# Kernel optimization log

Hardware: AMD Instinct MI355X
Metric: run time of the kernel (lower is better)

Reference implementation:

```python
import jax, jax.numpy as jnp
import numpy as np

N_NODES = 100000
N_HEDGES = 30000
N_PINS = 400000
D = 128          # hidden_channels
H = 4            # heads
K = D // H       # per-head dim
N_BLOCKS = 4     # n_layers=2, each layer = (vertex2edge, edge2vertex)
LN_EPS = 1e-5


def setup_inputs() -> dict:
    key = jax.random.key(0)
    ks = jax.random.split(key, 10)
    s = 1.0 / np.sqrt(D)
    return {
        "x_0": jax.random.normal(ks[0], (N_NODES, D), jnp.float32),
        "Kw": jax.random.normal(ks[1], (N_BLOCKS, H, D, K), jnp.float32) * s,
        "Vw": jax.random.normal(ks[2], (N_BLOCKS, H, D, K), jnp.float32) * s,
        "Qw": jax.random.normal(ks[3], (N_BLOCKS, H, K), jnp.float32) * s,
        "W1": jax.random.normal(ks[4], (N_BLOCKS, D, D), jnp.float32) * s,
        "b1": jnp.zeros((N_BLOCKS, D), jnp.float32),
        "W2": jax.random.normal(ks[5], (N_BLOCKS, D, D), jnp.float32) * s,
        "b2": jnp.zeros((N_BLOCKS, D), jnp.float32),
        "ln0_g": jnp.ones((N_BLOCKS, D), jnp.float32),
        "ln0_b": jnp.zeros((N_BLOCKS, D), jnp.float32),
        "ln1_g": jnp.ones((N_BLOCKS, D), jnp.float32),
        "ln1_b": jnp.zeros((N_BLOCKS, D), jnp.float32),
        "node_idx": jax.random.randint(ks[6], (N_PINS,), 0, N_NODES),
        "hedge_idx": jax.random.randint(ks[7], (N_PINS,), 0, N_HEDGES),
        "n_hyperedges": N_HEDGES,
    }


def _ln(x, g, b):
    mu = jnp.mean(x, -1, keepdims=True)
    var = jnp.mean((x - mu) ** 2, -1, keepdims=True)
    return (x - mu) * jax.lax.rsqrt(var + LN_EPS) * g + b


def _segment_softmax(logits, seg, num_segments):
    # softmax over incident pins grouped by target (sparse softmax over source dim)
    m = jax.ops.segment_max(logits, seg, num_segments=num_segments)
    ex = jnp.exp(logits - m[seg])
    denom = jax.ops.segment_sum(ex, seg, num_segments=num_segments)
    return ex / denom[seg]


def _block(x_src, src, tgt, n_tgt, Kw, Vw, Qw, W1, b1, W2, b2, g0, be0, g1, be1):
    # Multi-head PMA attention with a single learned query per head.
    Kx = jnp.einsum('nd,hdk->nhk', x_src, Kw)           # [n_src, H, K]
    Vx = jnp.einsum('nd,hdk->nhk', x_src, Vw)           # [n_src, H, K]
    logits = jnp.einsum('hk,nhk->nh', Qw, Kx)           # [n_src, H]
    w = _segment_softmax(logits[src], tgt, n_tgt)       # [E, H]
    msg = (w[:, :, None] * Vx[src]).reshape(-1, H * K)  # [E, D] head-concat
    agg = jax.ops.segment_sum(msg, tgt, num_segments=n_tgt)  # [n_tgt, D]
    x = _ln(agg + Qw.reshape(1, H * K), g0, be0)        # Q skip + LN0
    h = jnp.maximum(x @ W1 + b1, 0.0) @ W2 + b2         # 2-layer MLP
    return _ln(x + h, g1, be1)                          # residual + LN1


def reference(x_0, Kw, Vw, Qw, W1, b1, W2, b2, ln0_g, ln0_b, ln1_g, ln1_b,
              node_idx, hedge_idx, n_hyperedges):
    n_nodes = x_0.shape[0]
    x0, x1 = x_0, None
    for layer in range(N_BLOCKS // 2):
        bv, bev = 2 * layer, 2 * layer + 1
        # vertex -> hyperedge
        x1 = jax.nn.relu(_block(x0, node_idx, hedge_idx, n_hyperedges,
                                Kw[bv], Vw[bv], Qw[bv], W1[bv], b1[bv], W2[bv], b2[bv],
                                ln0_g[bv], ln0_b[bv], ln1_g[bv], ln1_b[bv]))
        # hyperedge -> vertex
        x0 = jax.nn.relu(_block(x1, hedge_idx, node_idx, n_nodes,
                                Kw[bev], Vw[bev], Qw[bev], W1[bev], b1[bev], W2[bev], b2[bev],
                                ln0_g[bev], ln0_b[bev], ln1_g[bev], ln1_b[bev]))
    return (x0, x1)
```

## Files before the change

kernel.cpp:

```cpp
#include <hip/hip_runtime.h>

#define N_NODES 100000
#define N_HEDGES 30000
#define N_PINS 400000
#define NPN 100096
#define NPH 30080
#define OVF_CAP 8192

typedef __attribute__((ext_vector_type(8))) short bf16x8;
typedef __attribute__((ext_vector_type(4))) float f32x4;
typedef unsigned short ushort_t;

__device__ __forceinline__ unsigned short f2bf(float f) {
  unsigned int u = __float_as_uint(f);
  u += 0x7FFF + ((u >> 16) & 1);
  return (unsigned short)(u >> 16);
}
__device__ __forceinline__ float bf2f(unsigned short s) {
  return __uint_as_float(((unsigned int)s) << 16);
}
__device__ __forceinline__ void gload16(const void* g, void* l) {
  __builtin_amdgcn_global_load_lds(
      (const __attribute__((address_space(1))) unsigned int*)g,
      (__attribute__((address_space(3))) unsigned int*)l, 16, 0, 0);
}

__global__ __launch_bounds__(256) void prep_k(
    const float* __restrict__ Kw, const float* __restrict__ Vw,
    const float* __restrict__ Qw, const float* __restrict__ W1,
    const float* __restrict__ W2, ushort_t* __restrict__ Vvqsw,
    ushort_t* __restrict__ W1sw, ushort_t* __restrict__ W2sw) {
  int i = blockIdx.x * 256 + threadIdx.x;
  if (i < 4 * 144 * 128) {
    int b = i / 18432, r = i % 18432, c = r >> 7, d = r & 127;
    float v;
    if (c < 128) {
      v = Vw[((b * 4 + (c >> 5)) * 128 + d) * 32 + (c & 31)];
    } else if (c < 132) {
      int h = c - 128;
      const float* kp = Kw + ((b * 4 + h) * 128 + d) * 32;
      const float* qp = Qw + (b * 4 + h) * 32;
      float s = 0.f;
      for (int k = 0; k < 32; ++k) s += kp[k] * qp[k];
      v = s;
    } else {
      v = 0.f;
    }
    int L = (c * 256 + d * 2) ^ ((c & 7) << 4);
    Vvqsw[b * 18432 + L / 2] = f2bf(v);
  }
  if (i < 4 * 128 * 128) {
    int b = i >> 14, r = i & 16383, c = r >> 7, k = r & 127;
    int L = (c * 256 + k * 2) ^ ((c & 7) << 4);
    int idx = b * 16384 + L / 2;
    W1sw[idx] = f2bf(W1[b * 16384 + k * 128 + c]);
    W2sw[idx] = f2bf(W2[b * 16384 + k * 128 + c]);
  }
}

__global__ __launch_bounds__(256) void conv_k(const float* __restrict__ x,
                                              ushort_t* __restrict__ xb, int n4) {
  int i = blockIdx.x * 256 + threadIdx.x;
  if (i < n4) {
    float4 v = ((const float4*)x)[i];
    ushort_t o0 = f2bf(v.x), o1 = f2bf(v.y), o2 = f2bf(v.z), o3 = f2bf(v.w);
    ushort_t* p = xb + (size_t)i * 4;
    p[0] = o0; p[1] = o1; p[2] = o2; p[3] = o3;
  }
}

__global__ __launch_bounds__(256) void csr_count(
    const int* __restrict__ node_idx, const int* __restrict__ hedge_idx,
    int* __restrict__ cntN, int* __restrict__ cntH) {
  int e = blockIdx.x * 256 + threadIdx.x;
  if (e < N_PINS) {
    atomicAdd(&cntN[node_idx[e]], 1);
    atomicAdd(&cntH[hedge_idx[e]], 1);
  }
}

__global__ __launch_bounds__(256) void csr_scan(
    const int* __restrict__ cnt, int* __restrict__ start, int2* __restrict__ seg,
    int n, int* gctr, int thresh, int* __restrict__ ovf, int* __restrict__ ovfcnt) {
  __shared__ int wsum[4];
  __shared__ int bbase;
  int i = blockIdx.x * 256 + threadIdx.x;
  int lane = threadIdx.x & 63, wid = threadIdx.x >> 6;
  int v = (i < n) ? cnt[i] : 0;
  int sc = v;
#pragma unroll
  for (int s = 1; s < 64; s <<= 1) {
    int tv = __shfl_up(sc, s);
    if (lane >= s) sc += tv;
  }
  if (lane == 63) wsum[wid] = sc;
  __syncthreads();
  if (threadIdx.x == 0) {
    int s0 = wsum[0], s1 = wsum[1], s2 = wsum[2], s3 = wsum[3];
    wsum[0] = 0; wsum[1] = s0; wsum[2] = s0 + s1; wsum[3] = s0 + s1 + s2;
    bbase = atomicAdd(gctr, s0 + s1 + s2 + s3);
  }
  __syncthreads();
  if (i < n) {
    int st = bbase + wsum[wid] + (sc - v);
    start[i] = st;
    seg[i] = make_int2(st, v);
    if (v > thresh) {
      int k = atomicAdd(ovfcnt, 1);
      if (k < OVF_CAP) ovf[k] = i;
    }
  }
}

__global__ __launch_bounds__(256) void csr_fill(
    const int* __restrict__ node_idx, const int* __restrict__ hedge_idx,
    const int* __restrict__ startN, const int* __restrict__ startH,
    int* __restrict__ fillN, int* __restrict__ fillH,
    int* __restrict__ pinsN, int* __restrict__ pinsH) {
  int e = blockIdx.x * 256 + threadIdx.x;
  if (e < N_PINS) {
    int n = node_idx[e], h = hedge_idx[e];
    int pH = startH[h] + atomicAdd(&fillH[h], 1);
    pinsH[pH] = n;
    int pN = startN[n] + atomicAdd(&fillN[n], 1);
    pinsN[pN] = h;
  }
}

__global__ __launch_bounds__(256) void transform_k(
    const ushort_t* __restrict__ xb, const ushort_t* __restrict__ Bsw,
    ushort_t* __restrict__ Vxb, float* __restrict__ lg, int n) {
  __shared__ char Blds[36864];
  __shared__ char Olds[16384];
  int t = threadIdx.x, l = t & 63, w = t >> 6;
  size_t r0 = (size_t)blockIdx.x * 64;
#pragma unroll
  for (int it = 0; it < 9; ++it) {
    int off = it * 4096 + w * 1024 + l * 16;
    gload16((const char*)Bsw + off, Blds + off);
  }
  __syncthreads();

  f32x4 acc[9];
#pragma unroll
  for (int ct = 0; ct < 9; ++ct) acc[ct] = (f32x4){0.f, 0.f, 0.f, 0.f};
  int swz = (l & 7) << 4;
  int lbase = (l & 15) * 256 + (l >> 4) * 16;
  const ushort_t* abase = xb + (r0 + w * 16 + (l & 15)) * 128 + (l >> 4) * 8;
#pragma unroll
  for (int kk = 0; kk < 4; ++kk) {
    bf16x8 a = *(const bf16x8*)(abase + kk * 32);
#pragma unroll
    for (int ct = 0; ct < 9; ++ct) {
      bf16x8 b = *(const bf16x8*)(Blds + ((ct * 4096 + kk * 64 + lbase) ^ swz));
      acc[ct] = __builtin_amdgcn_mfma_f32_16x16x32_bf16(a, b, acc[ct], 0, 0, 0);
    }
  }
  if ((l & 15) < 4) {
    size_t rb = r0 + w * 16 + (l >> 4) * 4;
#pragma unroll
    for (int j = 0; j < 4; ++j) lg[(rb + j) * 4 + (l & 15)] = acc[8][j];
  }
  int row64 = w * 16 + (l >> 4) * 4;
#pragma unroll
  for (int ct = 0; ct < 8; ++ct) {
    int c2 = (ct * 16 + (l & 15)) * 2;
#pragma unroll
    for (int j = 0; j < 4; ++j) {
      int r = row64 + j;
      int addr = (r * 256 + c2) ^ ((r & 0xC) << 3);
      *(ushort_t*)(Olds + addr) = f2bf(acc[ct][j]);
    }
  }
  __syncthreads();
#pragma unroll
  for (int it = 0; it < 4; ++it) {
    int L = it * 4096 + t * 16;
    int r = L >> 8;
    int phys = L ^ ((r & 0xC) << 3);
    *(uint4*)((char*)Vxb + r0 * 256 + L) = *(const uint4*)(Olds + phys);
  }
}

template <int L>
__global__ __launch_bounds__(256) void attn_g(
    const ushort_t* __restrict__ Vxb, const float* __restrict__ lg,
    const int2* __restrict__ seg, const int* __restrict__ pins,
    const float* __restrict__ Qflat, const float* __restrict__ g0,
    const float* __restrict__ be0, ushort_t* __restrict__ xmidb, int n_tgt,
    int mainBlocks, const int* __restrict__ ovf, const int* __restrict__ ovfcnt) {
  constexpr int G = 64 / L;
  constexpr int C = 128 / L;
  __shared__ float wl[4][G][L][4];
  __shared__ int pl[4][G][L];
  int wid = threadIdx.x >> 6, lane = threadIdx.x & 63;
  const char* vb = (const char*)Vxb;

  if ((int)blockIdx.x < mainBlocks) {
    int g = lane / L, li = lane % L;
    int tg = ((int)blockIdx.x * 4 + wid) * G + g;
    bool tval = tg < n_tgt;
    int2 sc = tval ? seg[tg] : make_int2(0, 0);
    int base = sc.x, deg = sc.y;
    bool fast = deg <= L;
    int mydeg = (tval && fast) ? deg : 0;
    bool act = li < mydeg;
    int p = act ? pins[base + li] : 0;
    float4 l4;
    if (act) l4 = *(const float4*)(lg + p * 4);
    else l4 = make_float4(-3.4e38f, -3.4e38f, -3.4e38f, -3.4e38f);
    float m0 = l4.x, m1 = l4.y, m2 = l4.z, m3 = l4.w;
#pragma unroll
    for (int off = 1; off < L; off <<= 1) {
      m0 = fmaxf(m0, __shfl_xor(m0, off));
      m1 = fmaxf(m1, __shfl_xor(m1, off));
      m2 = fmaxf(m2, __shfl_xor(m2, off));
      m3 = fmaxf(m3, __shfl_xor(m3, off));
    }
    float e0 = __expf(l4.x - m0), e1 = __expf(l4.y - m1);
    float e2 = __expf(l4.z - m2), e3 = __expf(l4.w - m3);
    float s0 = e0, s1 = e1, s2 = e2, s3 = e3;
#pragma unroll
    for (int off = 1; off < L; off <<= 1) {
      s0 += __shfl_xor(s0, off);
      s1 += __shfl_xor(s1, off);
      s2 += __shfl_xor(s2, off);
      s3 += __shfl_xor(s3, off);
    }
    wl[wid][g][li][0] = e0 / s0;
    wl[wid][g][li][1] = e1 / s1;
    wl[wid][g][li][2] = e2 / s2;
    wl[wid][g][li][3] = e3 / s3;
    pl[wid][g][li] = p << 8;

    int myh = li / (L / 4);
    float acc[C];
#pragma unroll
    for (int c = 0; c < C; ++c) acc[c] = 0.f;
    for (int e = 0; e < mydeg; ++e) {
      int off = pl[wid][g][e];
      float wgt = wl[wid][g][e][myh];
      const char* src = vb + off + li * (C * 2);
      unsigned u[C / 2];
      if constexpr (C == 8) {
        uint4 v = *(const uint4*)src;
        u[0] = v.x; u[1] = v.y; u[2] = v.z; u[3] = v.w;
      } else {
        uint2 v = *(const uint2*)src;
        u[0] = v.x; u[1] = v.y;
      }
#pragma unroll
      for (int j = 0; j < C / 2; ++j) {
        acc[2 * j] = fmaf(wgt, __uint_as_float(u[j] << 16), acc[2 * j]);
        acc[2 * j + 1] = fmaf(wgt, __uint_as_float(u[j] & 0xffff0000u), acc[2 * j + 1]);
      }
    }
    float q[C], gv[C], bv[C];
#pragma unroll
    for (int j = 0; j < C / 4; ++j) {
      float4 t = *(const float4*)(Qflat + li * C + j * 4);
      q[j * 4] = t.x; q[j * 4 + 1] = t.y; q[j * 4 + 2] = t.z; q[j * 4 + 3] = t.w;
      t = *(const float4*)(g0 + li * C + j * 4);
      gv[j * 4] = t.x; gv[j * 4 + 1] = t.y; gv[j * 4 + 2] = t.z; gv[j * 4 + 3] = t.w;
      t = *(const float4*)(be0 + li * C + j * 4);
      bv[j * 4] = t.x; bv[j * 4 + 1] = t.y; bv[j * 4 + 2] = t.z; bv[j * 4 + 3] = t.w;
    }
    float t1 = 0.f, t2 = 0.f;
#pragma unroll
    for (int c = 0; c < C; ++c) {
      float x = acc[c] + q[c];
      acc[c] = x;
      t1 += x;
      t2 += x * x;
    }
#pragma unroll
    for (int off = 1; off < L; off <<= 1) {
      t1 += __shfl_xor(t1, off);
      t2 += __shfl_xor(t2, off);
    }
    float mean = t1 * (1.f / 128.f);
    float var = t2 * (1.f / 128.f) - mean * mean;
    float rs = rsqrtf(var + 1e-5f);
    if (tval && fast) {
      float o[C];
#pragma unroll
      for (int c = 0; c < C; ++c) o[c] = (acc[c] - mean) * rs * gv[c] + bv[c];
      char* dst = (char*)xmidb + (size_t)tg * 256 + li * (C * 2);
      if constexpr (C == 8) {
        uint4 pk;
        pk.x = ((unsigned)f2bf(o[1]) << 16) | f2bf(o[0]);
        pk.y = ((unsigned)f2bf(o[3]) << 16) | f2bf(o[2]);
        pk.z = ((unsigned)f2bf(o[5]) << 16) | f2bf(o[4]);
        pk.w = ((unsigned)f2bf(o[7]) << 16) | f2bf(o[6]);
        *(uint4*)dst = pk;
      } else {
        uint2 pk;
        pk.x = ((unsigned)f2bf(o[1]) << 16) | f2bf(o[0]);
        pk.y = ((unsigned)f2bf(o[3]) << 16) | f2bf(o[2]);
        *(uint2*)dst = pk;
      }
    }
    return;
  }

  int cnt = *ovfcnt;
  if (cnt > OVF_CAP) cnt = OVF_CAP;
  int head = lane >> 4;
  for (int idx = ((int)blockIdx.x - mainBlocks) * 4 + wid; idx < cnt; idx += 128) {
    int tg = ovf[idx];
    int2 sc = seg[tg];
    int base = sc.x, deg = sc.y;
    float m0 = -3.4e38f, m1 = -3.4e38f, m2 = -3.4e38f, m3 = -3.4e38f;
    for (int i = lane; i < deg; i += 64) {
      int p = pins[base + i];
      float4 l4 = *(const float4*)(lg + p * 4);
      m0 = fmaxf(m0, l4.x); m1 = fmaxf(m1, l4.y);
      m2 = fmaxf(m2, l4.z); m3 = fmaxf(m3, l4.w);
    }
#pragma unroll
    for (int off = 1; off < 64; off <<= 1) {
      m0 = fmaxf(m0, __shfl_xor(m0, off));
      m1 = fmaxf(m1, __shfl_xor(m1, off));
      m2 = fmaxf(m2, __shfl_xor(m2, off));
      m3 = fmaxf(m3, __shfl_xor(m3, off));
    }
    float s0 = 0.f, s1 = 0.f, s2 = 0.f, s3 = 0.f;
    for (int i = lane; i < deg; i += 64) {
      int p = pins[base + i];
      float4 l4 = *(const float4*)(lg + p * 4);
      s0 += __expf(l4.x - m0); s1 += __expf(l4.y - m1);
      s2 += __expf(l4.z - m2); s3 += __expf(l4.w - m3);
    }
#pragma unroll
    for (int off = 1; off < 64; off <<= 1) {
      s0 += __shfl_xor(s0, off);
      s1 += __shfl_xor(s1, off);
      s2 += __shfl_xor(s2, off);
      s3 += __shfl_xor(s3, off);
    }
    float mh = (head & 2) ? ((head & 1) ? m3 : m2) : ((head & 1) ? m1 : m0);
    float sh = (head & 2) ? ((head & 1) ? s3 : s2) : ((head & 1) ? s1 : s0);
    float rdh = (deg > 0) ? 1.f / sh : 0.f;
    float acc0 = 0.f, acc1 = 0.f;
    for (int e = 0; e < deg; ++e) {
      int p = pins[base + e];
      float w0 = __expf(lg[p * 4 + head] - mh) * rdh;
      unsigned int v = *(const unsigned int*)(vb + (p << 8) + lane * 4);
      acc0 = fmaf(w0, __uint_as_float(v << 16), acc0);
      acc1 = fmaf(w0, __uint_as_float(v & 0xffff0000u), acc1);
    }
    float2 q2 = ((const float2*)Qflat)[lane];
    float x0v = acc0 + q2.x;
    float x1v = acc1 + q2.y;
    float t1 = x0v + x1v, t2 = x0v * x0v + x1v * x1v;
#pragma unroll
    for (int off = 1; off < 64; off <<= 1) {
      t1 += __shfl_xor(t1, off);
      t2 += __shfl_xor(t2, off);
    }
    float mean = t1 * (1.f / 128.f);
    float var = t2 * (1.f / 128.f) - mean * mean;
    float rs = rsqrtf(var + 1e-5f);
    float2 gg = ((const float2*)g0)[lane];
    float2 bb = ((const float2*)be0)[lane];
    float o0 = (x0v - mean) * rs * gg.x + bb.x;
    float o1 = (x1v - mean) * rs * gg.y + bb.y;
    unsigned int pk = ((unsigned int)f2bf(o1) << 16) | f2bf(o0);
    ((unsigned int*)xmidb)[tg * 64 + lane] = pk;
  }
}

__global__ __launch_bounds__(256) void mlp_k(
    const ushort_t* __restrict__ xmb, const ushort_t* __restrict__ W1sw,
    const float* __restrict__ b1, const ushort_t* __restrict__ W2sw,
    const float* __restrict__ b2, const float* __restrict__ g1,
    const float* __restrict__ be1, float* __restrict__ outf,
    ushort_t* __restrict__ outb, int n, int wf32) {
  __shared__ char Wlds[32768];
  __shared__ char Hlds[16384];
  int t = threadIdx.x, l = t & 63, w = t >> 6;
  size_t r0 = (size_t)blockIdx.x * 64;
#pragma unroll
  for (int it = 0; it < 8; ++it) {
    int off = it * 4096 + w * 1024 + l * 16;
    gload16((const char*)W1sw + off, Wlds + off);
  }
  float b1v[8], b2v[8], g1v[8], be1v[8];
#pragma unroll
  for (int ct = 0; ct < 8; ++ct) {
    int c = ct * 16 + (l & 15);
    b1v[ct] = b1[c]; b2v[ct] = b2[c]; g1v[ct] = g1[c]; be1v[ct] = be1[c];
  }
  __syncthreads();

  int swz = (l & 7) << 4;
  int lbase = (l & 15) * 256 + (l >> 4) * 16;
  f32x4 acc[8];
#pragma unroll
  for (int ct = 0; ct < 8; ++ct) acc[ct] = (f32x4){b1v[ct], b1v[ct], b1v[ct], b1v[ct]};
  const ushort_t* abase = xmb + (r0 + w * 16 + (l & 15)) * 128 + (l >> 4) * 8;
#pragma unroll
  for (int kk = 0; kk < 4; ++kk) {
    bf16x8 a = *(const bf16x8*)(abase + kk * 32);
#pragma unroll
    for (int ct = 0; ct < 8; ++ct) {
      bf16x8 b = *(const bf16x8*)(Wlds + ((ct * 4096 + kk * 64 + lbase) ^ swz));
      acc[ct] = __builtin_amdgcn_mfma_f32_16x16x32_bf16(a, b, acc[ct], 0, 0, 0);
    }
  }
  int hbase = w * 4096;
#pragma unroll
  for (int ct = 0; ct < 8; ++ct) {
    int c2 = (ct * 16 + (l & 15)) * 2;
#pragma unroll
    for (int j = 0; j < 4; ++j) {
      int rl = (l >> 4) * 4 + j;
      int addr = hbase + ((rl * 256 + c2) ^ ((rl & 7) << 4));
      *(ushort_t*)(Hlds + addr) = f2bf(fmaxf(acc[ct][j], 0.f));
    }
  }
  __syncthreads();
#pragma unroll
  for (int it = 0; it < 8; ++it) {
    int off = it * 4096 + w * 1024 + l * 16;
    gload16((const char*)W2sw + off, Wlds + off);
  }
  __syncthreads();

  f32x4 acc2[8];
#pragma unroll
  for (int ct = 0; ct < 8; ++ct) acc2[ct] = (f32x4){b2v[ct], b2v[ct], b2v[ct], b2v[ct]};
#pragma unroll
  for (int kk = 0; kk < 4; ++kk) {
    bf16x8 a = *(const bf16x8*)(Hlds + (hbase + ((lbase + kk * 64) ^ swz)));
#pragma unroll
    for (int ct = 0; ct < 8; ++ct) {
      bf16x8 b = *(const bf16x8*)(Wlds + ((ct * 4096 + kk * 64 + lbase) ^ swz));
      acc2[ct] = __builtin_amdgcn_mfma_f32_16x16x32_bf16(a, b, acc2[ct], 0, 0, 0);
    }
  }
  size_t rbase = r0 + w * 16 + (l >> 4) * 4;
  float s1[4] = {0.f, 0.f, 0.f, 0.f}, s2[4] = {0.f, 0.f, 0.f, 0.f};
#pragma unroll
  for (int ct = 0; ct < 8; ++ct) {
    int c = ct * 16 + (l & 15);
#pragma unroll
    for (int j = 0; j < 4; ++j) {
      float x = bf2f(xmb[(rbase + j) * 128 + c]);
      float y = acc2[ct][j] + x;
      acc2[ct][j] = y;
      s1[j] += y;
      s2[j] += y * y;
    }
  }
#pragma unroll
  for (int off = 1; off < 16; off <<= 1) {
#pragma unroll
    for (int j = 0; j < 4; ++j) {
      s1[j] += __shfl_xor(s1[j], off);
      s2[j] += __shfl_xor(s2[j], off);
    }
  }
  float mean[4], rs[4];
#pragma unroll
  for (int j = 0; j < 4; ++j) {
    mean[j] = s1[j] * (1.f / 128.f);
    float var = s2[j] * (1.f / 128.f) - mean[j] * mean[j];
    rs[j] = rsqrtf(var + 1e-5f);
  }
#pragma unroll
  for (int ct = 0; ct < 8; ++ct) {
    int c = ct * 16 + (l & 15);
#pragma unroll
    for (int j = 0; j < 4; ++j) {
      float o = fmaxf((acc2[ct][j] - mean[j]) * rs[j] * g1v[ct] + be1v[ct], 0.f);
      size_t row = rbase + j;
      outb[row * 128 + c] = f2bf(o);
      if (wf32 && row < (size_t)n) outf[row * 128 + c] = o;
    }
  }
}

extern "C" void kernel_launch(void* const* d_in, const int* in_sizes, int n_in,
                              void* d_out, int out_size, void* d_ws, size_t ws_size,
                              hipStream_t stream) {
  const float* x0_in = (const float*)d_in[0];
  const float* Kw  = (const float*)d_in[1];
  const float* Vw  = (const float*)d_in[2];
  const float* Qw  = (const float*)d_in[3];
  const float* W1  = (const float*)d_in[4];
  const float* b1  = (const float*)d_in[5];
  const float* W2  = (const float*)d_in[6];
  const float* b2  = (const float*)d_in[7];
  const float* ln0g = (const float*)d_in[8];
  const float* ln0b = (const float*)d_in[9];
  const float* ln1g = (const float*)d_in[10];
  const float* ln1b = (const float*)d_in[11];
  const int* node_idx  = (const int*)d_in[12];
  const int* hedge_idx = (const int*)d_in[13];

  float* out = (float*)d_out;
  float* x0_out = out;
  float* x1_out = out + (size_t)N_NODES * 128;

  char* w = (char*)d_ws;
  auto alloc = [&](size_t bytes) -> void* {
    void* p = (void*)w;
    w += (bytes + 255) & ~(size_t)255;
    return p;
  };
  ushort_t* Vvqsw = (ushort_t*)alloc(4 * 18432 * 2);
  ushort_t* W1sw  = (ushort_t*)alloc(4 * 16384 * 2);
  ushort_t* W2sw  = (ushort_t*)alloc(4 * 16384 * 2);
  ushort_t* x0b   = (ushort_t*)alloc((size_t)NPN * 128 * 2);
  ushort_t* x1b   = (ushort_t*)alloc((size_t)NPH * 128 * 2);
  ushort_t* Vxb   = (ushort_t*)alloc((size_t)NPN * 128 * 2);
  float*    lg    = (float*)alloc((size_t)NPN * 4 * 4);
  ushort_t* xmidb = (ushort_t*)alloc((size_t)NPN * 128 * 2);
  int* startH = (int*)alloc(N_HEDGES * 4);
  int* startN = (int*)alloc(N_NODES * 4);
  int2* segH  = (int2*)alloc((size_t)N_HEDGES * 8);
  int2* segN  = (int2*)alloc((size_t)N_NODES * 8);
  int* pinsH  = (int*)alloc(N_PINS * 4);
  int* pinsN  = (int*)alloc(N_PINS * 4);
  int* ovfH   = (int*)alloc(OVF_CAP * 4);
  int* ovfN   = (int*)alloc(OVF_CAP * 4);
  int* zbase  = (int*)alloc((size_t)(2 * (N_HEDGES + N_NODES) + 4) * 4);
  int* cntH = zbase;
  int* cntN = cntH + N_HEDGES;
  int* fillH = cntN + N_NODES;
  int* fillN = fillH + N_HEDGES;
  int* gctr = fillN + N_NODES;

  hipMemsetAsync(zbase, 0, (size_t)(2 * (N_HEDGES + N_NODES) + 4) * 4, stream);

  conv_k<<<(N_NODES * 128 / 4 + 255) / 256, 256, 0, stream>>>(x0_in, x0b, N_NODES * 32);
  prep_k<<<288, 256, 0, stream>>>(Kw, Vw, Qw, W1, W2, Vvqsw, W1sw, W2sw);
  csr_count<<<(N_PINS + 255) / 256, 256, 0, stream>>>(node_idx, hedge_idx, cntN, cntH);
  csr_scan<<<(N_HEDGES + 255) / 256, 256, 0, stream>>>(cntH, startH, segH, N_HEDGES,
                                                       gctr + 0, 32, ovfH, gctr + 2);
  csr_scan<<<(N_NODES + 255) / 256, 256, 0, stream>>>(cntN, startN, segN, N_NODES,
                                                      gctr + 1, 16, ovfN, gctr + 3);
  csr_fill<<<(N_PINS + 255) / 256, 256, 0, stream>>>(node_idx, hedge_idx, startN, startH,
                                                     fillN, fillH, pinsN, pinsH);

  const ushort_t* srcs[4] = {x0b, x1b, x0b, x1b};
  int n_srcs[4] = {N_NODES, N_HEDGES, N_NODES, N_HEDGES};
  const int2* segs[4] = {segH, segN, segH, segN};
  const int* pinss[4] = {pinsH, pinsN, pinsH, pinsN};
  int n_tgts[4] = {N_HEDGES, N_NODES, N_HEDGES, N_NODES};
  float* outf[4] = {x1_out, x0_out, x1_out, x0_out};
  ushort_t* outbs[4] = {x1b, x0b, x1b, x0b};
  int wf32[4] = {0, 0, 1, 1};

  const int mbH = (N_HEDGES + 7) / 8;
  const int mbN = (N_NODES + 15) / 16;

  for (int b = 0; b < 4; ++b) {
    int n_src = n_srcs[b], n_tgt = n_tgts[b];
    transform_k<<<(n_src + 63) / 64, 256, 0, stream>>>(srcs[b], Vvqsw + b * 18432,
                                                       Vxb, lg, n_src);
    if (b & 1) {
      attn_g<16><<<mbN + 32, 256, 0, stream>>>(Vxb, lg, segs[b], pinss[b],
                                               Qw + b * 128, ln0g + b * 128,
                                               ln0b + b * 128, xmidb, n_tgt,
                                               mbN, ovfN, gctr + 3);
    } else {
      attn_g<32><<<mbH + 32, 256, 0, stream>>>(Vxb, lg, segs[b], pinss[b],
                                               Qw + b * 128, ln0g + b * 128,
                                               ln0b + b * 128, xmidb, n_tgt,
                                               mbH, ovfH, gctr + 2);
    }
    mlp_k<<<(n_tgt + 63) / 64, 256, 0, stream>>>(xmidb, W1sw + b * 16384, b1 + b * 128,
                                                 W2sw + b * 16384, b2 + b * 128,
                                                 ln1g + b * 128, ln1b + b * 128,
                                                 outf[b], outbs[b], n_tgt, wf32[b]);
  }
}
```

Baseline: 315.6 us.

## Fuse preprocessing kernels and reuse count-atomic ranks for CSR fill

Merges the bf16 conversion, CSR counting and weight prep into one grid-stride kernel, and merges the two scans into one launch. The per-pin rank returned by the counting atomics is saved as a packed 16-bit pair, so the fill step no longer needs a second round of atomics or the fill counters. The last block also skips writing the unused bf16 output. This cuts launch count and atomic traffic. The packed ranks assume fewer than 65536 pins per segment.

```diff
diff --git a/kernel.cpp b/kernel.cpp
--- a/kernel.cpp
+++ b/kernel.cpp
@@ -6,6 +6,8 @@
 #define NPN 100096
 #define NPH 30080
 #define OVF_CAP 8192
+#define SCAN_BH 118
+#define SCAN_BN 391
 
 typedef __attribute__((ext_vector_type(8))) short bf16x8;
 typedef __attribute__((ext_vector_type(4))) float f32x4;
@@ -25,13 +27,28 @@
       (__attribute__((address_space(3))) unsigned int*)l, 16, 0, 0);
 }
 
-__global__ __launch_bounds__(256) void prep_k(
+__global__ __launch_bounds__(256) void fused_front(
+    const float* __restrict__ x0_in, ushort_t* __restrict__ x0b,
+    const int* __restrict__ node_idx, const int* __restrict__ hedge_idx,
+    int* __restrict__ cntN, int* __restrict__ cntH, unsigned* __restrict__ rank2,
     const float* __restrict__ Kw, const float* __restrict__ Vw,
     const float* __restrict__ Qw, const float* __restrict__ W1,
     const float* __restrict__ W2, ushort_t* __restrict__ Vvqsw,
     ushort_t* __restrict__ W1sw, ushort_t* __restrict__ W2sw) {
-  int i = blockIdx.x * 256 + threadIdx.x;
-  if (i < 4 * 144 * 128) {
+  int gsz = gridDim.x * 256;
+  int tid = blockIdx.x * 256 + threadIdx.x;
+  for (int i = tid; i < N_NODES * 32; i += gsz) {
+    float4 v = ((const float4*)x0_in)[i];
+    ushort_t* p = x0b + (size_t)i * 4;
+    p[0] = f2bf(v.x); p[1] = f2bf(v.y); p[2] = f2bf(v.z); p[3] = f2bf(v.w);
+  }
+  for (int e = tid; e < N_PINS; e += gsz) {
+    int n = node_idx[e], h = hedge_idx[e];
+    int rn = atomicAdd(&cntN[n], 1);
+    int rh = atomicAdd(&cntH[h], 1);
+    rank2[e] = ((unsigned)rh << 16) | (unsigned)rn;
+  }
+  for (int i = tid; i < 4 * 144 * 128; i += gsz) {
     int b = i / 18432, r = i % 18432, c = r >> 7, d = r & 127;
     float v;
     if (c < 128) {
@@ -49,7 +66,7 @@
     int L = (c * 256 + d * 2) ^ ((c & 7) << 4);
     Vvqsw[b * 18432 + L / 2] = f2bf(v);
   }
-  if (i < 4 * 128 * 128) {
+  for (int i = tid; i < 4 * 128 * 128; i += gsz) {
     int b = i >> 14, r = i & 16383, c = r >> 7, k = r & 127;
     int L = (c * 256 + k * 2) ^ ((c & 7) << 4);
     int idx = b * 16384 + L / 2;
@@ -58,33 +75,22 @@
   }
 }
 
-__global__ __launch_bounds__(256) void conv_k(const float* __restrict__ x,
-                                              ushort_t* __restrict__ xb, int n4) {
-  int i = blockIdx.x * 256 + threadIdx.x;
-  if (i < n4) {
-    float4 v = ((const float4*)x)[i];
-    ushort_t o0 = f2bf(v.x), o1 = f2bf(v.y), o2 = f2bf(v.z), o3 = f2bf(v.w);
-    ushort_t* p = xb + (size_t)i * 4;
-    p[0] = o0; p[1] = o1; p[2] = o2; p[3] = o3;
-  }
-}
-
-__global__ __launch_bounds__(256) void csr_count(
-    const int* __restrict__ node_idx, const int* __restrict__ hedge_idx,
-    int* __restrict__ cntN, int* __restrict__ cntH) {
-  int e = blockIdx.x * 256 + threadIdx.x;
-  if (e < N_PINS) {
-    atomicAdd(&cntN[node_idx[e]], 1);
-    atomicAdd(&cntH[hedge_idx[e]], 1);
-  }
-}
-
-__global__ __launch_bounds__(256) void csr_scan(
-    const int* __restrict__ cnt, int* __restrict__ start, int2* __restrict__ seg,
-    int n, int* gctr, int thresh, int* __restrict__ ovf, int* __restrict__ ovfcnt) {
+__global__ __launch_bounds__(256) void csr_scan2(
+    const int* __restrict__ cntH, int* __restrict__ startH, int2* __restrict__ segH,
+    int* __restrict__ ovfH, const int* __restrict__ cntN, int* __restrict__ startN,
+    int2* __restrict__ segN, int* __restrict__ ovfN, int* __restrict__ gctr) {
   __shared__ int wsum[4];
   __shared__ int bbase;
-  int i = blockIdx.x * 256 + threadIdx.x;
+  bool isH = (int)blockIdx.x < SCAN_BH;
+  const int* cnt = isH ? cntH : cntN;
+  int* start = isH ? startH : startN;
+  int2* seg = isH ? segH : segN;
+  int* ovf = isH ? ovfH : ovfN;
+  int* g = gctr + (isH ? 0 : 1);
+  int* oc = gctr + (isH ? 2 : 3);
+  int thresh = isH ? 32 : 16;
+  int n = isH ? N_HEDGES : N_NODES;
+  int i = (isH ? (int)blockIdx.x : (int)blockIdx.x - SCAN_BH) * 256 + threadIdx.x;
   int lane = threadIdx.x & 63, wid = threadIdx.x >> 6;
   int v = (i < n) ? cnt[i] : 0;
   int sc = v;
@@ -98,7 +104,7 @@
   if (threadIdx.x == 0) {
     int s0 = wsum[0], s1 = wsum[1], s2 = wsum[2], s3 = wsum[3];
     wsum[0] = 0; wsum[1] = s0; wsum[2] = s0 + s1; wsum[3] = s0 + s1 + s2;
-    bbase = atomicAdd(gctr, s0 + s1 + s2 + s3);
+    bbase = atomicAdd(g, s0 + s1 + s2 + s3);
   }
   __syncthreads();
   if (i < n) {
@@ -106,7 +112,7 @@
     start[i] = st;
     seg[i] = make_int2(st, v);
     if (v > thresh) {
-      int k = atomicAdd(ovfcnt, 1);
+      int k = atomicAdd(oc, 1);
       if (k < OVF_CAP) ovf[k] = i;
     }
   }
@@ -114,16 +120,15 @@
 
 __global__ __launch_bounds__(256) void csr_fill(
     const int* __restrict__ node_idx, const int* __restrict__ hedge_idx,
-    const int* __restrict__ startN, const int* __restrict__ startH,
-    int* __restrict__ fillN, int* __restrict__ fillH,
-    int* __restrict__ pinsN, int* __restrict__ pinsH) {
+    const unsigned* __restrict__ rank2, const int* __restrict__ startN,
+    const int* __restrict__ startH, int* __restrict__ pinsN,
+    int* __restrict__ pinsH) {
   int e = blockIdx.x * 256 + threadIdx.x;
   if (e < N_PINS) {
     int n = node_idx[e], h = hedge_idx[e];
-    int pH = startH[h] + atomicAdd(&fillH[h], 1);
-    pinsH[pH] = n;
-    int pN = startN[n] + atomicAdd(&fillN[n], 1);
-    pinsN[pN] = h;
+    unsigned r2 = rank2[e];
+    pinsH[startH[h] + (int)(r2 >> 16)] = n;
+    pinsN[startN[n] + (int)(r2 & 0xffffu)] = h;
   }
 }
 
@@ -375,7 +380,7 @@
     const float* __restrict__ b1, const ushort_t* __restrict__ W2sw,
     const float* __restrict__ b2, const float* __restrict__ g1,
     const float* __restrict__ be1, float* __restrict__ outf,
-    ushort_t* __restrict__ outb, int n, int wf32) {
+    ushort_t* __restrict__ outb, int n, int flags) {
   __shared__ char Wlds[32768];
   __shared__ char Hlds[16384];
   int t = threadIdx.x, l = t & 63, w = t >> 6;
@@ -475,8 +480,8 @@
     for (int j = 0; j < 4; ++j) {
       float o = fmaxf((acc2[ct][j] - mean[j]) * rs[j] * g1v[ct] + be1v[ct], 0.f);
       size_t row = rbase + j;
-      outb[row * 128 + c] = f2bf(o);
-      if (wf32 && row < (size_t)n) outf[row * 128 + c] = o;
+      if (flags & 2) outb[row * 128 + c] = f2bf(o);
+      if ((flags & 1) && row < (size_t)n) outf[row * 128 + c] = o;
     }
   }
 }
@@ -525,24 +530,20 @@
   int* pinsN  = (int*)alloc(N_PINS * 4);
   int* ovfH   = (int*)alloc(OVF_CAP * 4);
   int* ovfN   = (int*)alloc(OVF_CAP * 4);
-  int* zbase  = (int*)alloc((size_t)(2 * (N_HEDGES + N_NODES) + 4) * 4);
+  unsigned* rank2 = (unsigned*)alloc((size_t)N_PINS * 4);
+  int* zbase  = (int*)alloc((size_t)(N_HEDGES + N_NODES + 4) * 4);
   int* cntH = zbase;
   int* cntN = cntH + N_HEDGES;
-  int* fillH = cntN + N_NODES;
-  int* fillN = fillH + N_HEDGES;
-  int* gctr = fillN + N_NODES;
-
-  hipMemsetAsync(zbase, 0, (size_t)(2 * (N_HEDGES + N_NODES) + 4) * 4, stream);
-
-  conv_k<<<(N_NODES * 128 / 4 + 255) / 256, 256, 0, stream>>>(x0_in, x0b, N_NODES * 32);
-  prep_k<<<288, 256, 0, stream>>>(Kw, Vw, Qw, W1, W2, Vvqsw, W1sw, W2sw);
-  csr_count<<<(N_PINS + 255) / 256, 256, 0, stream>>>(node_idx, hedge_idx, cntN, cntH);
-  csr_scan<<<(N_HEDGES + 255) / 256, 256, 0, stream>>>(cntH, startH, segH, N_HEDGES,
-                                                       gctr + 0, 32, ovfH, gctr + 2);
-  csr_scan<<<(N_NODES + 255) / 256, 256, 0, stream>>>(cntN, startN, segN, N_NODES,
-                                                      gctr + 1, 16, ovfN, gctr + 3);
-  csr_fill<<<(N_PINS + 255) / 256, 256, 0, stream>>>(node_idx, hedge_idx, startN, startH,
-                                                     fillN, fillH, pinsN, pinsH);
+  int* gctr = cntN + N_NODES;
+
+  hipMemsetAsync(zbase, 0, (size_t)(N_HEDGES + N_NODES + 4) * 4, stream);
+
+  fused_front<<<1024, 256, 0, stream>>>(x0_in, x0b, node_idx, hedge_idx, cntN, cntH,
+                                        rank2, Kw, Vw, Qw, W1, W2, Vvqsw, W1sw, W2sw);
+  csr_scan2<<<SCAN_BH + SCAN_BN, 256, 0, stream>>>(cntH, startH, segH, ovfH,
+                                                   cntN, startN, segN, ovfN, gctr);
+  csr_fill<<<(N_PINS + 255) / 256, 256, 0, stream>>>(node_idx, hedge_idx, rank2,
+                                                     startN, startH, pinsN, pinsH);
 
   const ushort_t* srcs[4] = {x0b, x1b, x0b, x1b};
   int n_srcs[4] = {N_NODES, N_HEDGES, N_NODES, N_HEDGES};
@@ -551,7 +552,7 @@
   int n_tgts[4] = {N_HEDGES, N_NODES, N_HEDGES, N_NODES};
   float* outf[4] = {x1_out, x0_out, x1_out, x0_out};
   ushort_t* outbs[4] = {x1b, x0b, x1b, x0b};
-  int wf32[4] = {0, 0, 1, 1};
+  int flags[4] = {2, 2, 3, 1};
 
   const int mbH = (N_HEDGES + 7) / 8;
   const int mbN = (N_NODES + 15) / 16;
@@ -574,6 +575,6 @@
     mlp_k<<<(n_tgt + 63) / 64, 256, 0, stream>>>(xmidb, W1sw + b * 16384, b1 + b * 128,
                                                  W2sw + b * 16384, b2 + b * 128,
                                                  ln1g + b * 128, ln1b + b * 128,
-                                                 outf[b], outbs[b], n_tgt, wf32[b]);
-  }
-}
+                                                 outf[b], outbs[b], n_tgt, flags[b]);
+  }
+}
```

New measurement: 289.1 us. -8.4%, faster.
